# Optimization experiments

Measured on AMD Instinct MI355X. Metric: run time of the kernel, lower is better.

The kernel has to match this reference:

```python
import jax, jax.numpy as jnp
import numpy as np

B, T, C = 2, 2048, 1024
H = 16
D = C // H  # 64

def setup_inputs() -> dict:
    key = jax.random.key(0)
    k1, k2, k3 = jax.random.split(key, 3)
    s = 0.02
    return {
        "x": jax.random.normal(k1, (B, T, C), dtype=jnp.float32),
        "Wqkv": jax.random.normal(k2, (C, 3 * C), dtype=jnp.float32) * s,
        "bqkv": jnp.zeros((3 * C,), dtype=jnp.float32),
        "Wproj": jax.random.normal(k3, (C, C), dtype=jnp.float32) * s,
        "bproj": jnp.zeros((C,), dtype=jnp.float32),
    }

def reference(x, Wqkv, bqkv, Wproj, bproj):
    b, t, c = x.shape
    qkv = x @ Wqkv + bqkv                       # [B,T,3C]
    qkv = qkv.reshape(b, t, 3, H, D)
    q = qkv[:, :, 0].transpose(0, 2, 1, 3)      # [B,H,T,D]
    k = qkv[:, :, 1].transpose(0, 2, 1, 3)
    v = qkv[:, :, 2].transpose(0, 2, 1, 3)
    scale = 1.0 / np.sqrt(D).astype(np.float32)
    att = jnp.einsum('bhqd,bhkd->bhqk', q, k) * scale  # [B,H,T,T]
    causal = jnp.tril(jnp.ones((t, t), dtype=bool))
    att = jnp.where(causal[None, None], att, jnp.float32(-jnp.inf))
    att = jax.nn.softmax(att, axis=-1)
    y = jnp.einsum('bhqk,bhkd->bhqd', att, v)   # [B,H,T,D]
    y = y.transpose(0, 2, 1, 3).reshape(b, t, c)
    return y @ Wproj + bproj
```

## Files before the change

### kernel.cpp

```cpp
#include <hip/hip_runtime.h>

typedef __bf16 bf16x8 __attribute__((ext_vector_type(8)));
typedef float  f32x4  __attribute__((ext_vector_type(4)));
typedef float  f32x16 __attribute__((ext_vector_type(16)));
typedef unsigned int uint32x4 __attribute__((ext_vector_type(4)));

__device__ __forceinline__ short f2bf(float f) {
  union { float f; unsigned u; } v; v.f = f;
  unsigned r = v.u + 0x7fffu + ((v.u >> 16) & 1u);
  return (short)(r >> 16);
}

__device__ __forceinline__ void gl_lds16(const short* g, short* l) {
  __builtin_amdgcn_global_load_lds((const __attribute__((address_space(1))) void*)g,
                                   (__attribute__((address_space(3))) void*)l, 16, 0, 0);
}

__global__ __launch_bounds__(256) void cast_x_kernel(const float* __restrict__ in,
                                                     short* __restrict__ out, int n4) {
  int i = blockIdx.x * 256 + threadIdx.x;
  if (i >= n4) return;
  float4 f = reinterpret_cast<const float4*>(in)[i];
  short4 o;
  o.x = f2bf(f.x); o.y = f2bf(f.y); o.z = f2bf(f.z); o.w = f2bf(f.w);
  reinterpret_cast<short4*>(out)[i] = o;
}

__global__ __launch_bounds__(256) void transpose_cast(const float* __restrict__ in,
                                                      short* __restrict__ out, int R, int Cc) {
  __shared__ short tile[64][65];
  int bx = blockIdx.x * 64;
  int by = blockIdx.y * 64;
  int tx = threadIdx.x & 63, ty = threadIdx.x >> 6;
  #pragma unroll
  for (int i = ty; i < 64; i += 4)
    tile[i][tx] = f2bf(in[(size_t)(by + i) * Cc + bx + tx]);
  __syncthreads();
  #pragma unroll
  for (int i = ty; i < 64; i += 4)
    out[(size_t)(bx + i) * R + by + tx] = tile[tx][i];
}


__global__ __launch_bounds__(512, 1) void gemm_qkv(const short* __restrict__ A,
                                                   const short* __restrict__ Bt,
                                                   const float* __restrict__ bias,
                                                   short* __restrict__ qo,
                                                   short* __restrict__ ko,
                                                   short* __restrict__ vt) {
  const int K = 1024;
  __shared__ short smem[65536];
  int tid = threadIdx.x;
  int x = blockIdx.x & 7, r = blockIdx.x >> 3;
  int mtile = (x * 2 + (r & 1)) * 256;
  int ntile = (r >> 1) * 256;
  int w = tid >> 6, l = tid & 63;
  int wr = w >> 2, wc = w & 3;
  int lr = l & 15, lg = l >> 4;

  f32x4 zero4 = {0.f, 0.f, 0.f, 0.f};
  f32x4 acc[8][4];
  #pragma unroll
  for (int i = 0; i < 8; ++i)
    #pragma unroll
    for (int j = 0; j < 4; ++j) acc[i][j] = zero4;

#define STAGE_QKV(BUF, K0) do {                                                      \
    short* Ab_ = smem + (BUF) * 32768;                                               \
    short* Bb_ = Ab_ + 16384;                                                        \
    _Pragma("unroll")                                                                \
    for (int c = 0; c < 4; ++c) {                                                    \
      int idx = tid + c * 512;                                                       \
      int row = idx >> 3, kc = (idx & 7) ^ (row & 7);       \
      gl_lds16(&A[(size_t)(mtile + row) * K + (K0) + kc * 8], &Ab_[idx * 8]);        \
      gl_lds16(&Bt[(size_t)(ntile + row) * K + (K0) + kc * 8], &Bb_[idx * 8]);       \
    }                                                                                \
  } while (0)

  STAGE_QKV(0, 0);
  __syncthreads();
  int cur = 0;
  for (int it = 0; it < 16; ++it) {
    if (it < 15) STAGE_QKV(cur ^ 1, (it + 1) * 64);
    const short* Ab = smem + cur * 32768;
    const short* Bb = Ab + 16384;
    __builtin_amdgcn_s_setprio(1);
    #pragma unroll
    for (int kk = 0; kk < 2; ++kk) {
      bf16x8 af[8], bfr[4];
      #pragma unroll
      for (int i = 0; i < 8; ++i) {
        int rA = wr * 128 + i * 16 + lr;
        af[i] = *reinterpret_cast<const bf16x8*>(&Ab[rA * 64 + (((kk * 4 + lg) ^ (rA & 7)) * 8)]);
      }
      #pragma unroll
      for (int j = 0; j < 4; ++j) {
        int rB = wc * 64 + j * 16 + lr;
        bfr[j] = *reinterpret_cast<const bf16x8*>(&Bb[rB * 64 + (((kk * 4 + lg) ^ (rB & 7)) * 8)]);
      }
      #pragma unroll
      for (int i = 0; i < 8; ++i)
        #pragma unroll
        for (int j = 0; j < 4; ++j)
          acc[i][j] = __builtin_amdgcn_mfma_f32_16x16x32_bf16(af[i], bfr[j], acc[i][j], 0, 0, 0);
    }
    __builtin_amdgcn_s_setprio(0);
    __syncthreads();
    cur ^= 1;
  }
#undef STAGE_QKV

  const int sec = ntile >> 10;
  if (sec == 2) {
    #pragma unroll
    for (int j = 0; j < 4; ++j) {
      int nl = wc * 64 + j * 16 + lr;
      int d  = nl & 63;
      float bv = bias[ntile + nl];
      #pragma unroll
      for (int i = 0; i < 8; ++i) {
        int lt0 = wr * 128 + i * 16 + lg * 4;
        int c2 = (nl >> 6) * 8 + (lt0 >> 5);
        int pos = (((lt0 >> 3) & 1) << 10) + (d & 31) * 32 +
                  ((((lt0 >> 4) & 1) + ((d >> 5) << 1)) << 3) + (lt0 & 7);
        short4 pk;
        pk.x = f2bf(acc[i][j][0] + bv);
        pk.y = f2bf(acc[i][j][1] + bv);
        pk.z = f2bf(acc[i][j][2] + bv);
        pk.w = f2bf(acc[i][j][3] + bv);
        *reinterpret_cast<short4*>(&smem[c2 * 2048 + pos]) = pk;
      }
    }
  } else {
    const float sc = (sec == 0) ? 0.18033688f : 1.0f;
    #pragma unroll
    for (int j = 0; j < 4; ++j) {
      int nl = wc * 64 + j * 16 + lr;
      int d  = nl & 63;
      float bv = bias[ntile + nl];
      int dpart = (((d >> 3) & 1) << 10) + ((d >> 4) << 3) + (d & 7);
      #pragma unroll
      for (int i = 0; i < 8; ++i) {
        #pragma unroll
        for (int r2 = 0; r2 < 4; ++r2) {
          int lt = wr * 128 + i * 16 + lg * 4 + r2;
          int c2 = (nl >> 6) * 8 + (lt >> 5);
          smem[c2 * 2048 + (lt & 31) * 32 + dpart] = f2bf((acc[i][j][r2] + bv) * sc);
        }
      }
    }
  }
  __syncthreads();
  short* dst = (sec == 0) ? qo : ((sec == 1) ? ko : vt);
  int bb  = mtile >> 11;
  int h0  = (ntile & 1023) >> 6;
  int gt0 = (mtile & 2047) >> 5;
  #pragma unroll
  for (int c2 = 0; c2 < 32; ++c2) {
    size_t base = (size_t)(bb * 16 + h0 + (c2 >> 3)) * 131072 +
                  (size_t)(gt0 + (c2 & 7)) * 2048;
    *reinterpret_cast<uint2*>(&dst[base + tid * 4]) =
        *reinterpret_cast<const uint2*>(&smem[c2 * 2048 + tid * 4]);
  }
}

template<int DIAG>
__device__ __forceinline__ void attn_step(const short* __restrict__ kp,
                                          const short* __restrict__ vp,
                                          const bf16x8* qf,
                                          f32x16& y0, f32x16& y1,
                                          float& m, float& li,
                                          int lq, int hl) {
  f32x16 s;
  #pragma unroll
  for (int r = 0; r < 16; ++r) s[r] = -m;
  __builtin_amdgcn_s_setprio(1);
  #pragma unroll
  for (int ks = 0; ks < 4; ++ks) {
    bf16x8 kf = *reinterpret_cast<const bf16x8*>(kp + ks * 8);
    s = __builtin_amdgcn_mfma_f32_32x32x16_bf16(kf, qf[ks], s, 0, 0, 0);
  }
  __builtin_amdgcn_s_setprio(0);
  if (DIAG) {
    #pragma unroll
    for (int r = 0; r < 16; ++r) {
      int kvl = (r & 3) + 8 * (r >> 2) + 4 * hl;
      if (kvl > lq) s[r] = -1e30f;
    }
  }
  float t0 = fmaxf(fmaxf(s[0], s[1]), s[2]);
  float t1 = fmaxf(fmaxf(s[3], s[4]), s[5]);
  float t2 = fmaxf(fmaxf(s[6], s[7]), s[8]);
  float t3 = fmaxf(fmaxf(s[9], s[10]), s[11]);
  float t4 = fmaxf(fmaxf(s[12], s[13]), s[14]);
  float pm = fmaxf(fmaxf(fmaxf(t0, t1), t2), fmaxf(fmaxf(t3, t4), s[15]));
  if (!__all(pm <= 8.0f)) {
    float pmu = fmaxf(pm, __shfl_xor(pm, 32));
    float delta = fmaxf(pmu, 0.0f);
    float sc = __builtin_amdgcn_exp2f(-delta);
    m += delta;
    li *= sc;
    #pragma unroll
    for (int r = 0; r < 16; ++r) { y0[r] *= sc; y1[r] *= sc; s[r] -= delta; }
  }
  unsigned u[8];
  float rs = 0.f;
  #pragma unroll
  for (int rq = 0; rq < 4; ++rq) {
    float p0 = __builtin_amdgcn_exp2f(s[4 * rq + 0]);
    float p1 = __builtin_amdgcn_exp2f(s[4 * rq + 1]);
    float p2 = __builtin_amdgcn_exp2f(s[4 * rq + 2]);
    float p3 = __builtin_amdgcn_exp2f(s[4 * rq + 3]);
    rs += (p0 + p1) + (p2 + p3);
    asm("v_cvt_pk_bf16_f32 %0, %1, %2" : "=v"(u[rq * 2 + 0]) : "v"(p0), "v"(p1));
    asm("v_cvt_pk_bf16_f32 %0, %1, %2" : "=v"(u[rq * 2 + 1]) : "v"(p2), "v"(p3));
  }
  li += rs;
  asm volatile("v_permlane32_swap_b32 %0, %1" : "+v"(u[0]), "+v"(u[2]));
  asm volatile("v_permlane32_swap_b32 %0, %1" : "+v"(u[1]), "+v"(u[3]));
  asm volatile("v_permlane32_swap_b32 %0, %1" : "+v"(u[4]), "+v"(u[6]));
  asm volatile("v_permlane32_swap_b32 %0, %1" : "+v"(u[5]), "+v"(u[7]));
  uint32x4 w0 = {u[0], u[1], u[2], u[3]};
  uint32x4 w1 = {u[4], u[5], u[6], u[7]};
  bf16x8 pa0 = __builtin_bit_cast(bf16x8, w0);
  bf16x8 pa1 = __builtin_bit_cast(bf16x8, w1);
  __builtin_amdgcn_s_setprio(1);
  {
    bf16x8 vf00 = *reinterpret_cast<const bf16x8*>(vp);
    bf16x8 vf01 = *reinterpret_cast<const bf16x8*>(vp + 8);
    bf16x8 vf10 = *reinterpret_cast<const bf16x8*>(vp + 16);
    bf16x8 vf11 = *reinterpret_cast<const bf16x8*>(vp + 24);
    y0 = __builtin_amdgcn_mfma_f32_32x32x16_bf16(vf00, pa0, y0, 0, 0, 0);
    y0 = __builtin_amdgcn_mfma_f32_32x32x16_bf16(vf01, pa1, y0, 0, 0, 0);
    y1 = __builtin_amdgcn_mfma_f32_32x32x16_bf16(vf10, pa0, y1, 0, 0, 0);
    y1 = __builtin_amdgcn_mfma_f32_32x32x16_bf16(vf11, pa1, y1, 0, 0, 0);
  }
  __builtin_amdgcn_s_setprio(0);
}

__global__ __launch_bounds__(256, 4) void attn_kernel(const short* __restrict__ q,
                                                      const short* __restrict__ k,
                                                      const short* __restrict__ vt,
                                                      short* __restrict__ y) {
  __shared__ float partL[3][4][64][4];
  __shared__ float stm[4][32], stl[4][32];
  const int bid = blockIdx.x;
  const int p = bid >> 5;
  const int b5 = bid & 31;
  const int bh = (b5 & 7) * 4 + (b5 >> 3);
  const int tid = threadIdx.x;
  const int w = tid >> 6;
  const int l = tid & 63;
  const int lq = l & 31, hl = l >> 5;
  const short* qb = q + (size_t)bh * 131072;
  const short* kb = k + (size_t)bh * 131072;
  const short* vb = vt + (size_t)bh * 131072;
  const int b_ = bh >> 4, h_ = bh & 15;

  #pragma unroll 1
  for (int half = 0; half < 2; ++half) {
    const int t = half ? p : (63 - p);

    bf16x8 qf[4];
    {
      const short* qp = qb + (size_t)t * 2048 + l * 32;
      #pragma unroll
      for (int ks = 0; ks < 4; ++ks)
        qf[ks] = *reinterpret_cast<const bf16x8*>(qp + ks * 8);
    }

    f32x16 y0, y1;
    #pragma unroll
    for (int r = 0; r < 16; ++r) { y0[r] = 0.f; y1[r] = 0.f; }
    float m = 0.f, li = 0.f;

    const short* kp = kb + (size_t)w * 2048 + l * 32;
    const short* vp = vb + (size_t)w * 2048 + l * 32;
    for (int it = w; it < t; it += 4) {
      attn_step<0>(kp, vp, qf, y0, y1, m, li, lq, hl);
      kp += 4 * 2048;
      vp += 4 * 2048;
    }
    if ((t & 3) == w) {
      const short* kpd = kb + (size_t)t * 2048 + l * 32;
      const short* vpd = vb + (size_t)t * 2048 + l * 32;
      attn_step<1>(kpd, vpd, qf, y0, y1, m, li, lq, hl);
    }
    li += __shfl_xor(li, 32);

    if (hl == 0) { stm[w][lq] = m; stl[w][lq] = li; }
    __syncthreads();
    float m0 = stm[0][lq], m1 = stm[1][lq], m2 = stm[2][lq], m3 = stm[3][lq];
    float M = fmaxf(fmaxf(m0, m1), fmaxf(m2, m3));
    float L = stl[0][lq] * __builtin_amdgcn_exp2f(m0 - M) +
              stl[1][lq] * __builtin_amdgcn_exp2f(m1 - M) +
              stl[2][lq] * __builtin_amdgcn_exp2f(m2 - M) +
              stl[3][lq] * __builtin_amdgcn_exp2f(m3 - M);
    float sc = __builtin_amdgcn_exp2f(m - M);
    #pragma unroll
    for (int r = 0; r < 16; ++r) { y0[r] *= sc; y1[r] *= sc; }

    if (w > 0) {
      #pragma unroll
      for (int c = 0; c < 4; ++c) {
        f32x4 v0s = {y0[4 * c + 0], y0[4 * c + 1], y0[4 * c + 2], y0[4 * c + 3]};
        *reinterpret_cast<f32x4*>(&partL[w - 1][c][l][0]) = v0s;
      }
    }
    __syncthreads();
    if (w == 0) {
      #pragma unroll
      for (int o = 0; o < 3; ++o)
        #pragma unroll
        for (int c = 0; c < 4; ++c) {
          f32x4 v0s = *reinterpret_cast<const f32x4*>(&partL[o][c][l][0]);
          #pragma unroll
          for (int r = 0; r < 4; ++r) y0[4 * c + r] += v0s[r];
        }
    }
    __syncthreads();
    if (w > 0) {
      #pragma unroll
      for (int c = 0; c < 4; ++c) {
        f32x4 v1s = {y1[4 * c + 0], y1[4 * c + 1], y1[4 * c + 2], y1[4 * c + 3]};
        *reinterpret_cast<f32x4*>(&partL[w - 1][c][l][0]) = v1s;
      }
    }
    __syncthreads();
    if (w == 0) {
      #pragma unroll
      for (int o = 0; o < 3; ++o)
        #pragma unroll
        for (int c = 0; c < 4; ++c) {
          f32x4 v1s = *reinterpret_cast<const f32x4*>(&partL[o][c][l][0]);
          #pragma unroll
          for (int r = 0; r < 4; ++r) y1[4 * c + r] += v1s[r];
        }
      float inv = 1.0f / L;
      short* yrow = &y[(size_t)(b_ * 2048 + 32 * t + lq) * 1024 + h_ * 64];
      #pragma unroll
      for (int dt = 0; dt < 2; ++dt) {
        const f32x16& yy = dt ? y1 : y0;
        #pragma unroll
        for (int rq = 0; rq < 4; ++rq) {
          int d0 = dt * 32 + 8 * rq + 4 * hl;
          uint2 pk;
          pk.x = (unsigned)(unsigned short)f2bf(yy[4 * rq + 0] * inv) |
                 ((unsigned)(unsigned short)f2bf(yy[4 * rq + 1] * inv) << 16);
          pk.y = (unsigned)(unsigned short)f2bf(yy[4 * rq + 2] * inv) |
                 ((unsigned)(unsigned short)f2bf(yy[4 * rq + 3] * inv) << 16);
          *reinterpret_cast<uint2*>(yrow + d0) = pk;
        }
      }
    }
    __syncthreads();
  }
}

__global__ __launch_bounds__(256, 3) void gemm_proj(const short* __restrict__ A,
                                                    const short* __restrict__ Bt,
                                                    const float* __restrict__ bias,
                                                    float* __restrict__ out) {
  const int K = 1024;
  __shared__ short smem[24576];
  int tid = threadIdx.x;
  int x = blockIdx.x & 7, r = blockIdx.x >> 3;
  int ntile = (x * 2 + (r & 1)) * 64, mtile = (r >> 1) * 128;
  int w = tid >> 6, l = tid & 63;
  int lr = l & 15, lg = l >> 4;

  f32x4 zero4 = {0.f, 0.f, 0.f, 0.f};
  f32x4 acc[2][4];
  #pragma unroll
  for (int i = 0; i < 2; ++i)
    #pragma unroll
    for (int j = 0; j < 4; ++j) acc[i][j] = zero4;

#define STAGE_PRJ(BUF, K0) do {                                                      \
    short* Ab_ = smem + (BUF) * 12288;                                               \
    short* Bb_ = Ab_ + 8192;                                                         \
    _Pragma("unroll")                                                                \
    for (int c = 0; c < 4; ++c) {                                                    \
      int idx = tid + c * 256;                                                       \
      int row = idx >> 3, kc = (idx & 7) ^ (row & 7);                                \
      gl_lds16(&A[(size_t)(mtile + row) * K + (K0) + kc * 8], &Ab_[idx * 8]);        \
    }                                                                                \
    _Pragma("unroll")                                                                \
    for (int c = 0; c < 2; ++c) {                                                    \
      int idx = tid + c * 256;                                                       \
      int row = idx >> 3, kc = (idx & 7) ^ (row & 7);                                \
      gl_lds16(&Bt[(size_t)(ntile + row) * K + (K0) + kc * 8], &Bb_[idx * 8]);       \
    }                                                                                \
  } while (0)

  STAGE_PRJ(0, 0);
  __syncthreads();
  int cur = 0;
  for (int it = 0; it < 16; ++it) {
    if (it < 15) STAGE_PRJ(cur ^ 1, (it + 1) * 64);
    const short* Ab = smem + cur * 12288;
    const short* Bb = Ab + 8192;
    __builtin_amdgcn_s_setprio(1);
    #pragma unroll
    for (int kk = 0; kk < 2; ++kk) {
      bf16x8 af[2], bfr[4];
      #pragma unroll
      for (int i = 0; i < 2; ++i) {
        int rA = w * 32 + i * 16 + lr;
        af[i] = *reinterpret_cast<const bf16x8*>(&Ab[rA * 64 + (((kk * 4 + lg) ^ (rA & 7)) * 8)]);
      }
      #pragma unroll
      for (int j = 0; j < 4; ++j) {
        int rB = j * 16 + lr;
        bfr[j] = *reinterpret_cast<const bf16x8*>(&Bb[rB * 64 + (((kk * 4 + lg) ^ (rB & 7)) * 8)]);
      }
      #pragma unroll
      for (int i = 0; i < 2; ++i)
        #pragma unroll
        for (int j = 0; j < 4; ++j)
          acc[i][j] = __builtin_amdgcn_mfma_f32_16x16x32_bf16(af[i], bfr[j], acc[i][j], 0, 0, 0);
    }
    __builtin_amdgcn_s_setprio(0);
    __syncthreads();
    cur ^= 1;
  }
#undef STAGE_PRJ

  #pragma unroll
  for (int j = 0; j < 4; ++j) {
    int n = ntile + j * 16 + lr;
    float bv = bias[n];
    #pragma unroll
    for (int i = 0; i < 2; ++i) {
      #pragma unroll
      for (int r2 = 0; r2 < 4; ++r2) {
        int m = mtile + w * 32 + i * 16 + lg * 4 + r2;
        out[(size_t)m * 1024 + n] = acc[i][j][r2] + bv;
      }
    }
  }
}

extern "C" void kernel_launch(void* const* d_in, const int* in_sizes, int n_in,
                              void* d_out, int out_size, void* d_ws, size_t ws_size,
                              hipStream_t stream) {
  const float* x     = (const float*)d_in[0];
  const float* Wqkv  = (const float*)d_in[1];
  const float* bqkv  = (const float*)d_in[2];
  const float* Wproj = (const float*)d_in[3];
  const float* bproj = (const float*)d_in[4];
  float* out = (float*)d_out;

  const size_t M4 = 4096ull * 1024ull;
  short* ws = (short*)d_ws;
  short* x_bf    = ws;
  short* wqkv_t  = ws + M4;
  short* wproj_t = ws + M4 + 3ull * 1024 * 1024;
  short* qb      = wproj_t + 1024ull * 1024;
  short* kb      = qb + M4;
  short* vtb     = kb + M4;
  short* yb      = x_bf;

  cast_x_kernel<<<4096, 256, 0, stream>>>(x, x_bf, (int)(M4 / 4));
  transpose_cast<<<dim3(48, 16), 256, 0, stream>>>(Wqkv, wqkv_t, 1024, 3072);
  transpose_cast<<<dim3(16, 16), 256, 0, stream>>>(Wproj, wproj_t, 1024, 1024);
  gemm_qkv<<<192, 512, 0, stream>>>(x_bf, wqkv_t, bqkv, qb, kb, vtb);
  attn_kernel<<<1024, 256, 0, stream>>>(qb, kb, vtb, yb);
  gemm_proj<<<512, 256, 0, stream>>>(yb, wproj_t, bproj, out);
}
```

Before: 110.6 us.

## Share KV tiles via double-buffered LDS across four query tiles per block

The attention kernel changes from splitting one query tile's KV range across four waves (then merging partial softmax states through LDS) to giving each wave its own query tile. Each block now owns four adjacent query tiles. K and V tiles are staged once into double-buffered, XOR-swizzled LDS with async global-to-LDS loads and shared by all four waves. This removes the cross-wave softmax merge and cuts redundant global K/V reads. In exchange it adds a barrier per KV step, cuts the grid from 1024 to 256 blocks with lower occupancy, and leaves waves with shorter causal ranges idle while the last wave finishes.

```diff
diff --git a/kernel.cpp b/kernel.cpp
--- a/kernel.cpp
+++ b/kernel.cpp
@@ -165,19 +165,19 @@
 }
 
 template<int DIAG>
-__device__ __forceinline__ void attn_step(const short* __restrict__ kp,
-                                          const short* __restrict__ vp,
+__device__ __forceinline__ void attn_step(const short* __restrict__ Kb,
+                                          const short* __restrict__ Vb,
                                           const bf16x8* qf,
                                           f32x16& y0, f32x16& y1,
                                           float& m, float& li,
-                                          int lq, int hl) {
+                                          int lq, int hl, int l) {
   f32x16 s;
   #pragma unroll
   for (int r = 0; r < 16; ++r) s[r] = -m;
   __builtin_amdgcn_s_setprio(1);
   #pragma unroll
   for (int ks = 0; ks < 4; ++ks) {
-    bf16x8 kf = *reinterpret_cast<const bf16x8*>(kp + ks * 8);
+    bf16x8 kf = *reinterpret_cast<const bf16x8*>(&Kb[l * 32 + ((ks ^ ((l >> 1) & 3)) * 8)]);
     s = __builtin_amdgcn_mfma_f32_32x32x16_bf16(kf, qf[ks], s, 0, 0, 0);
   }
   __builtin_amdgcn_s_setprio(0);
@@ -226,44 +226,53 @@
   bf16x8 pa1 = __builtin_bit_cast(bf16x8, w1);
   __builtin_amdgcn_s_setprio(1);
   {
-    bf16x8 vf00 = *reinterpret_cast<const bf16x8*>(vp);
-    bf16x8 vf01 = *reinterpret_cast<const bf16x8*>(vp + 8);
-    bf16x8 vf10 = *reinterpret_cast<const bf16x8*>(vp + 16);
-    bf16x8 vf11 = *reinterpret_cast<const bf16x8*>(vp + 24);
-    y0 = __builtin_amdgcn_mfma_f32_32x32x16_bf16(vf00, pa0, y0, 0, 0, 0);
-    y0 = __builtin_amdgcn_mfma_f32_32x32x16_bf16(vf01, pa1, y0, 0, 0, 0);
-    y1 = __builtin_amdgcn_mfma_f32_32x32x16_bf16(vf10, pa0, y1, 0, 0, 0);
-    y1 = __builtin_amdgcn_mfma_f32_32x32x16_bf16(vf11, pa1, y1, 0, 0, 0);
+    bf16x8 vf0 = *reinterpret_cast<const bf16x8*>(&Vb[l * 32 + ((0 ^ ((l >> 1) & 3)) * 8)]);
+    bf16x8 vf1 = *reinterpret_cast<const bf16x8*>(&Vb[l * 32 + ((1 ^ ((l >> 1) & 3)) * 8)]);
+    bf16x8 vf2 = *reinterpret_cast<const bf16x8*>(&Vb[l * 32 + ((2 ^ ((l >> 1) & 3)) * 8)]);
+    bf16x8 vf3 = *reinterpret_cast<const bf16x8*>(&Vb[l * 32 + ((3 ^ ((l >> 1) & 3)) * 8)]);
+    y0 = __builtin_amdgcn_mfma_f32_32x32x16_bf16(vf0, pa0, y0, 0, 0, 0);
+    y0 = __builtin_amdgcn_mfma_f32_32x32x16_bf16(vf1, pa1, y0, 0, 0, 0);
+    y1 = __builtin_amdgcn_mfma_f32_32x32x16_bf16(vf2, pa0, y1, 0, 0, 0);
+    y1 = __builtin_amdgcn_mfma_f32_32x32x16_bf16(vf3, pa1, y1, 0, 0, 0);
   }
   __builtin_amdgcn_s_setprio(0);
 }
 
-__global__ __launch_bounds__(256, 4) void attn_kernel(const short* __restrict__ q,
+__global__ __launch_bounds__(256, 2) void attn_kernel(const short* __restrict__ q,
                                                       const short* __restrict__ k,
                                                       const short* __restrict__ vt,
                                                       short* __restrict__ y) {
-  __shared__ float partL[3][4][64][4];
-  __shared__ float stm[4][32], stl[4][32];
+  __shared__ short Ks[2][2048];
+  __shared__ short Vs[2][2048];
   const int bid = blockIdx.x;
   const int p = bid >> 5;
   const int b5 = bid & 31;
   const int bh = (b5 & 7) * 4 + (b5 >> 3);
   const int tid = threadIdx.x;
-  const int w = tid >> 6;
-  const int l = tid & 63;
+  const int w = tid >> 6, l = tid & 63;
   const int lq = l & 31, hl = l >> 5;
   const short* qb = q + (size_t)bh * 131072;
   const short* kb = k + (size_t)bh * 131072;
   const short* vb = vt + (size_t)bh * 131072;
   const int b_ = bh >> 4, h_ = bh & 15;
 
+  const int sks = (tid & 3) ^ ((tid >> 3) & 3);
+  const int soff = (tid >> 2) * 32 + sks * 8;
+
+#define STAGE_ATT(BUF, TILE) do {                                          \
+    gl_lds16(kb + (size_t)(TILE) * 2048 + soff, &Ks[BUF][tid * 8]);        \
+    gl_lds16(vb + (size_t)(TILE) * 2048 + soff, &Vs[BUF][tid * 8]);        \
+  } while (0)
+
   #pragma unroll 1
   for (int half = 0; half < 2; ++half) {
-    const int t = half ? p : (63 - p);
+    const int base = half ? (60 - 4 * p) : 4 * p;
+    const int tq = base + w;
+    const int nt = base + 4;
 
     bf16x8 qf[4];
     {
-      const short* qp = qb + (size_t)t * 2048 + l * 32;
+      const short* qp = qb + (size_t)tq * 2048 + l * 32;
       #pragma unroll
       for (int ks = 0; ks < 4; ++ks)
         qf[ks] = *reinterpret_cast<const bf16x8*>(qp + ks * 8);
@@ -274,87 +283,38 @@
     for (int r = 0; r < 16; ++r) { y0[r] = 0.f; y1[r] = 0.f; }
     float m = 0.f, li = 0.f;
 
-    const short* kp = kb + (size_t)w * 2048 + l * 32;
-    const short* vp = vb + (size_t)w * 2048 + l * 32;
-    for (int it = w; it < t; it += 4) {
-      attn_step<0>(kp, vp, qf, y0, y1, m, li, lq, hl);
-      kp += 4 * 2048;
-      vp += 4 * 2048;
-    }
-    if ((t & 3) == w) {
-      const short* kpd = kb + (size_t)t * 2048 + l * 32;
-      const short* vpd = vb + (size_t)t * 2048 + l * 32;
-      attn_step<1>(kpd, vpd, qf, y0, y1, m, li, lq, hl);
+    STAGE_ATT(0, 0);
+    __syncthreads();
+    int buf = 0;
+    for (int it = 0; it < nt; ++it) {
+      if (it + 1 < nt) STAGE_ATT(buf ^ 1, it + 1);
+      if (it < tq)
+        attn_step<0>(&Ks[buf][0], &Vs[buf][0], qf, y0, y1, m, li, lq, hl, l);
+      else if (it == tq)
+        attn_step<1>(&Ks[buf][0], &Vs[buf][0], qf, y0, y1, m, li, lq, hl, l);
+      __syncthreads();
+      buf ^= 1;
     }
     li += __shfl_xor(li, 32);
 
-    if (hl == 0) { stm[w][lq] = m; stl[w][lq] = li; }
-    __syncthreads();
-    float m0 = stm[0][lq], m1 = stm[1][lq], m2 = stm[2][lq], m3 = stm[3][lq];
-    float M = fmaxf(fmaxf(m0, m1), fmaxf(m2, m3));
-    float L = stl[0][lq] * __builtin_amdgcn_exp2f(m0 - M) +
-              stl[1][lq] * __builtin_amdgcn_exp2f(m1 - M) +
-              stl[2][lq] * __builtin_amdgcn_exp2f(m2 - M) +
-              stl[3][lq] * __builtin_amdgcn_exp2f(m3 - M);
-    float sc = __builtin_amdgcn_exp2f(m - M);
-    #pragma unroll
-    for (int r = 0; r < 16; ++r) { y0[r] *= sc; y1[r] *= sc; }
-
-    if (w > 0) {
-      #pragma unroll
-      for (int c = 0; c < 4; ++c) {
-        f32x4 v0s = {y0[4 * c + 0], y0[4 * c + 1], y0[4 * c + 2], y0[4 * c + 3]};
-        *reinterpret_cast<f32x4*>(&partL[w - 1][c][l][0]) = v0s;
-      }
-    }
-    __syncthreads();
-    if (w == 0) {
-      #pragma unroll
-      for (int o = 0; o < 3; ++o)
-        #pragma unroll
-        for (int c = 0; c < 4; ++c) {
-          f32x4 v0s = *reinterpret_cast<const f32x4*>(&partL[o][c][l][0]);
-          #pragma unroll
-          for (int r = 0; r < 4; ++r) y0[4 * c + r] += v0s[r];
-        }
-    }
-    __syncthreads();
-    if (w > 0) {
-      #pragma unroll
-      for (int c = 0; c < 4; ++c) {
-        f32x4 v1s = {y1[4 * c + 0], y1[4 * c + 1], y1[4 * c + 2], y1[4 * c + 3]};
-        *reinterpret_cast<f32x4*>(&partL[w - 1][c][l][0]) = v1s;
-      }
-    }
-    __syncthreads();
-    if (w == 0) {
-      #pragma unroll
-      for (int o = 0; o < 3; ++o)
-        #pragma unroll
-        for (int c = 0; c < 4; ++c) {
-          f32x4 v1s = *reinterpret_cast<const f32x4*>(&partL[o][c][l][0]);
-          #pragma unroll
-          for (int r = 0; r < 4; ++r) y1[4 * c + r] += v1s[r];
-        }
-      float inv = 1.0f / L;
-      short* yrow = &y[(size_t)(b_ * 2048 + 32 * t + lq) * 1024 + h_ * 64];
-      #pragma unroll
-      for (int dt = 0; dt < 2; ++dt) {
-        const f32x16& yy = dt ? y1 : y0;
-        #pragma unroll
-        for (int rq = 0; rq < 4; ++rq) {
-          int d0 = dt * 32 + 8 * rq + 4 * hl;
-          uint2 pk;
-          pk.x = (unsigned)(unsigned short)f2bf(yy[4 * rq + 0] * inv) |
-                 ((unsigned)(unsigned short)f2bf(yy[4 * rq + 1] * inv) << 16);
-          pk.y = (unsigned)(unsigned short)f2bf(yy[4 * rq + 2] * inv) |
-                 ((unsigned)(unsigned short)f2bf(yy[4 * rq + 3] * inv) << 16);
-          *reinterpret_cast<uint2*>(yrow + d0) = pk;
-        }
-      }
-    }
-    __syncthreads();
-  }
+    float inv = 1.0f / li;
+    short* yrow = &y[(size_t)(b_ * 2048 + 32 * tq + lq) * 1024 + h_ * 64];
+    #pragma unroll
+    for (int dt = 0; dt < 2; ++dt) {
+      const f32x16& yy = dt ? y1 : y0;
+      #pragma unroll
+      for (int rq = 0; rq < 4; ++rq) {
+        int d0 = dt * 32 + 8 * rq + 4 * hl;
+        uint2 pk;
+        pk.x = (unsigned)(unsigned short)f2bf(yy[4 * rq + 0] * inv) |
+               ((unsigned)(unsigned short)f2bf(yy[4 * rq + 1] * inv) << 16);
+        pk.y = (unsigned)(unsigned short)f2bf(yy[4 * rq + 2] * inv) |
+               ((unsigned)(unsigned short)f2bf(yy[4 * rq + 3] * inv) << 16);
+        *reinterpret_cast<uint2*>(yrow + d0) = pk;
+      }
+    }
+  }
+#undef STAGE_ATT
 }
 
 __global__ __launch_bounds__(256, 3) void gemm_proj(const short* __restrict__ A,
@@ -465,6 +425,6 @@
   transpose_cast<<<dim3(48, 16), 256, 0, stream>>>(Wqkv, wqkv_t, 1024, 3072);
   transpose_cast<<<dim3(16, 16), 256, 0, stream>>>(Wproj, wproj_t, 1024, 1024);
   gemm_qkv<<<192, 512, 0, stream>>>(x_bf, wqkv_t, bqkv, qb, kb, vtb);
-  attn_kernel<<<1024, 256, 0, stream>>>(qb, kb, vtb, yb);
+  attn_kernel<<<256, 256, 0, stream>>>(qb, kb, vtb, yb);
   gemm_proj<<<512, 256, 0, stream>>>(yb, wproj_t, bproj, out);
 }
```

Result: slower. 119.3 us (+7.9%).
